# Kernel tuning notes

Hardware: AMD Instinct MI355X
Metric: run time of the kernel (lower is better)

The kernel has to match this reference:

```python
import jax, jax.numpy as jnp
import numpy as np

B, N, IN_DIM, DIM, HEADS, P = 4, 2048, 256, 512, 8, 16
DH = DIM // HEADS            # 64
SCALE = DH ** -0.5


def setup_inputs() -> dict:
    key = jax.random.key(0)
    ks = jax.random.split(key, 8)
    def w(k, shape, s=0.02):
        return jax.random.normal(k, shape, dtype=jnp.float32) * s
    return {
        "x": jax.random.normal(ks[0], (B, N, IN_DIM), dtype=jnp.float32),
        "w_qkv": w(ks[1], (IN_DIM, 3 * DIM)),
        "b_qkv": jnp.zeros((3 * DIM,), jnp.float32),
        "w_in": w(ks[2], (P, P)),
        "b_in": jnp.zeros((P,), jnp.float32),
        "w_out": w(ks[3], (P, P)),
        "b_out": jnp.zeros((P,), jnp.float32),
        "w_merge": w(ks[4], (DIM, DIM)),
        "b_merge": jnp.zeros((DIM,), jnp.float32),
        "w_proj": w(ks[5], (DIM + IN_DIM, DIM)),
        "b_proj": jnp.zeros((DIM,), jnp.float32),
        "H": 64,
        "W": 32,
    }


def reference(x, w_qkv, b_qkv, w_in, b_in, w_out, b_out,
              w_merge, b_merge, w_proj, b_proj, H, W):
    b, n, _ = x.shape
    qkv = x @ w_qkv + b_qkv                      # [b, n, 3*DIM]
    q, k, v = jnp.split(qkv, 3, axis=-1)
    def to_heads(t):
        return t.reshape(b, n, HEADS, DH).transpose(0, 2, 1, 3)  # [b, h, n, d]
    q, k, v = to_heads(q), to_heads(k), to_heads(v)
    # Original splits heads into h/v halves and runs two attentions, then
    # concats along the head axis. Softmax is per-head, so this is exactly
    # one batched multi-head attention with head order preserved.
    attn = jax.nn.softmax(jnp.einsum('bhnd,bhmd->bhnm', q, k) * SCALE, axis=-1)
    out = jnp.einsum('bhnm,bhmd->bhnd', attn, v)
    out = out.transpose(0, 2, 1, 3).reshape(b, n, DIM)
    out = out @ w_merge + b_merge
    # IBPP branch: view channels as [P, P] grid, linear-SiLU-linear on last dim
    xr = x.reshape(b, n, P, P)
    ib = jax.nn.silu(xr @ w_in + b_in) @ w_out + b_out
    ib = ib.reshape(b, n, IN_DIM)
    # proj (dropout p=0 -> identity)
    return jnp.concatenate([out, ib], axis=-1) @ w_proj + b_proj
```

## Files before the change

### kernel.cpp

```cpp
#include <hip/hip_runtime.h>


typedef unsigned short u16;
typedef unsigned int u32;
typedef __bf16 bf16x8 __attribute__((ext_vector_type(8)));
typedef u16 su16x8 __attribute__((ext_vector_type(8)));
typedef u16 su16x4 __attribute__((ext_vector_type(4)));
typedef u32 u32x4 __attribute__((ext_vector_type(4)));
typedef float f32x4 __attribute__((ext_vector_type(4)));
typedef float f32x16 __attribute__((ext_vector_type(16)));

__device__ __forceinline__ u16 f2bf(float f) {
  union { __bf16 h; u16 u; } v;
  v.h = (__bf16)f;
  return v.u;
}

__device__ __forceinline__ float fexp2(float x) {
#if __has_builtin(__builtin_amdgcn_exp2f)
  return __builtin_amdgcn_exp2f(x);
#else
  return __expf(x * 0.6931471805599453f);
#endif
}

__device__ __forceinline__ f32x4 zero4() {
  f32x4 v = {0.f, 0.f, 0.f, 0.f};
  return v;
}

__device__ __forceinline__ f32x4 mfma16(bf16x8 a, bf16x8 b, f32x4 c) {
  return __builtin_amdgcn_mfma_f32_16x16x32_bf16(a, b, c, 0, 0, 0);
}

__device__ __forceinline__ f32x16 mfma32(bf16x8 a, bf16x8 b, f32x16 c) {
  return __builtin_amdgcn_mfma_f32_32x32x16_bf16(a, b, c, 0, 0, 0);
}

__device__ __forceinline__ u32 pkbf(float a, float b) {
  u32 r;
  asm("v_cvt_pk_bf16_f32 %0, %1, %2" : "=v"(r) : "v"(a), "v"(b));
  return r;
}

__device__ __forceinline__ void swap32(u32& a, u32& b) {
  asm("v_permlane32_swap_b32 %0, %1" : "+v"(a), "+v"(b));
}

__device__ __forceinline__ bf16x8 mkfrag(u32 w0, u32 w1, u32 w2, u32 w3) {
  union { u32 u[4]; bf16x8 v; } x;
  x.u[0] = w0; x.u[1] = w1; x.u[2] = w2; x.u[3] = w3;
  return x.v;
}

__global__ __launch_bounds__(256) void prep_kernel(
    const float* __restrict__ w_qkv, const float* __restrict__ w_merge,
    const float* __restrict__ w_proj, const float* __restrict__ b_merge,
    const float* __restrict__ b_proj, u16* __restrict__ wqkvT,
    u16* __restrict__ wptT, u16* __restrict__ wcombT, u16* __restrict__ wmb,
    float* __restrict__ biasc) {
  int blk = blockIdx.x, tid = threadIdx.x;
  if (blk < 192) {
    const float* src;
    int lsrc, ldd, r0, c0;
    u16* dst;
    if (blk < 96) {
      src = w_qkv; lsrc = 1536; dst = wqkvT; ldd = 256;
      r0 = (blk & 3) * 64; c0 = (blk >> 2) * 64;
    } else if (blk < 160) {
      int b2 = blk - 96;
      src = w_proj; lsrc = 512; dst = wptT; ldd = 512;
      r0 = (b2 & 7) * 64; c0 = (b2 >> 3) * 64;
    } else {
      int b2 = blk - 160;
      src = w_proj + 512 * 512; lsrc = 512; dst = wcombT + 512; ldd = 768;
      r0 = (b2 & 3) * 64; c0 = (b2 >> 2) * 64;
    }
    __shared__ __align__(16) u16 Ts[64 * 68];
    int rr = tid >> 4, cc4 = (tid & 15) * 4;
#pragma unroll
    for (int rep = 0; rep < 4; ++rep) {
      int r = rr + rep * 16;
      float4 v = *(const float4*)&src[(size_t)(r0 + r) * lsrc + c0 + cc4];
      su16x4 pk = {f2bf(v.x), f2bf(v.y), f2bf(v.z), f2bf(v.w)};
      *(su16x4*)&Ts[r * 68 + cc4] = pk;
    }
    __syncthreads();
    int c = tid & 63, seg = tid >> 6;
    u16 tmp[16];
#pragma unroll
    for (int k = 0; k < 16; ++k) tmp[k] = Ts[(seg * 16 + k) * 68 + c];
    *(su16x8*)&dst[(size_t)(c0 + c) * ldd + r0 + seg * 16] = *(su16x8*)tmp;
    *(su16x8*)&dst[(size_t)(c0 + c) * ldd + r0 + seg * 16 + 8] =
        *(su16x8*)(tmp + 8);
  } else if (blk < 256) {
    int b2 = blk - 192;
#pragma unroll
    for (int rep = 0; rep < 4; ++rep) {
      int i = b2 * 4096 + rep * 1024 + tid * 4;
      float4 v = *(const float4*)&w_merge[i];
      su16x4 pk = {f2bf(v.x), f2bf(v.y), f2bf(v.z), f2bf(v.w)};
      *(su16x4*)&wmb[i] = pk;
    }
  } else {
    int col0 = (blk - 256) * 16;
    __shared__ float red[16][17];
    int kr = tid >> 4, cc = tid & 15;
    float s = 0.f;
#pragma unroll 4
    for (int j = 0; j < 32; ++j) {
      int k = kr + j * 16;
      s += b_merge[k] * w_proj[(size_t)k * 512 + col0 + cc];
    }
    red[kr][cc] = s;
    __syncthreads();
    if (kr == 0) {
      float a = b_proj[col0 + cc];
#pragma unroll
      for (int t = 0; t < 16; ++t) a += red[t][cc];
      biasc[col0 + cc] = a;
    }
  }
}

__global__ __launch_bounds__(256) void ib_kernel(
    const float* __restrict__ x, const float* __restrict__ w_in,
    const float* __restrict__ b_in, const float* __restrict__ w_out,
    const float* __restrict__ b_out, u16* __restrict__ xb,
    u16* __restrict__ catb) {
  __shared__ float wi[256], wo[256], bi[16], bo[16];
  __shared__ float xs[16][260];
  __shared__ float hs[16][260];
  int tid = threadIdx.x;
  wi[tid] = w_in[tid];
  wo[tid] = w_out[tid];
  if (tid < 16) { bi[tid] = b_in[tid]; bo[tid] = b_out[tid]; }
  size_t blkoff = (size_t)blockIdx.x * 4096;
#pragma unroll
  for (int i = 0; i < 4; ++i) {
    int f = (tid + i * 256) * 4;
    float4 v = *(const float4*)&x[blkoff + f];
    int tok = f >> 8, p = f & 255;
    *(float4*)&xs[tok][p] = v;
    su16x4 pk = {f2bf(v.x), f2bf(v.y), f2bf(v.z), f2bf(v.w)};
    *(su16x4*)&xb[blkoff + f] = pk;
  }
  __syncthreads();
  int t = tid >> 4, p2 = tid & 15;
#pragma unroll
  for (int p1 = 0; p1 < 16; ++p1) {
    float a = bi[p2];
#pragma unroll
    for (int k = 0; k < 16; ++k) a += xs[t][p1 * 16 + k] * wi[k * 16 + p2];
    hs[t][p1 * 16 + p2] = a / (1.f + __expf(-a));
  }
  __syncthreads();
  size_t tok = (size_t)blockIdx.x * 16 + t;
#pragma unroll
  for (int p1 = 0; p1 < 16; ++p1) {
    float o = bo[p2];
#pragma unroll
    for (int j = 0; j < 16; ++j) o += hs[t][p1 * 16 + j] * wo[j * 16 + p2];
    catb[tok * 768 + 512 + p1 * 16 + p2] = f2bf(o);
  }
}

template <int TM, int TN, int WGM, int WGN, int OUTMODE>
__global__ __launch_bounds__(256) void gemm_bt(
    const u16* __restrict__ A, int lda, const u16* __restrict__ BT, int ldb,
    int kcount, const float* __restrict__ bias, void* __restrict__ Co, int ldc,
    int scaleQ) {
  constexpr int NROWS = TM + TN;
  constexpr int NLD = NROWS / 64;
  constexpr int MT = TM / WGM / 16;
  constexpr int NT = TN / WGN / 16;
  __shared__ __align__(16) u16 S[NROWS * 40];
  int tid = threadIdx.x;
  int lane = tid & 63, wave = tid >> 6;
  int c = lane & 15, g4 = lane >> 4;
  int m0 = blockIdx.y * TM, n0 = blockIdx.x * TN;
  int wm = (wave / WGN) * (TM / WGM), wn = (wave % WGN) * (TN / WGN);
  f32x4 acc[MT][NT];
#pragma unroll
  for (int a = 0; a < MT; ++a)
#pragma unroll
    for (int b = 0; b < NT; ++b) acc[a][b] = zero4();

  su16x8 pre[NLD];
#pragma unroll
  for (int t = 0; t < NLD; ++t) {
    int gsl = t * 256 + tid;
    int row = gsl >> 2, kg = gsl & 3;
    const u16* p = row < TM ? &A[(size_t)(m0 + row) * lda + kg * 8]
                            : &BT[(size_t)(n0 + row - TM) * ldb + kg * 8];
    pre[t] = *(const su16x8*)p;
  }

  for (int kb = 0; kb < kcount; kb += 32) {
    __syncthreads();
#pragma unroll
    for (int t = 0; t < NLD; ++t) {
      int gsl = t * 256 + tid;
      int row = gsl >> 2, kg = gsl & 3;
      *(su16x8*)&S[row * 40 + kg * 8] = pre[t];
    }
    __syncthreads();
    if (kb + 32 < kcount) {
#pragma unroll
      for (int t = 0; t < NLD; ++t) {
        int gsl = t * 256 + tid;
        int row = gsl >> 2, kg = gsl & 3;
        const u16* p =
            row < TM ? &A[(size_t)(m0 + row) * lda + kb + 32 + kg * 8]
                     : &BT[(size_t)(n0 + row - TM) * ldb + kb + 32 + kg * 8];
        pre[t] = *(const su16x8*)p;
      }
    }
    bf16x8 af[MT], bf[NT];
#pragma unroll
    for (int mt = 0; mt < MT; ++mt)
      af[mt] = *(const bf16x8*)&S[(wm + mt * 16 + c) * 40 + g4 * 8];
#pragma unroll
    for (int nt = 0; nt < NT; ++nt)
      bf[nt] = *(const bf16x8*)&S[(TM + wn + nt * 16 + c) * 40 + g4 * 8];
#pragma unroll
    for (int mt = 0; mt < MT; ++mt)
#pragma unroll
      for (int nt = 0; nt < NT; ++nt)
        acc[mt][nt] = mfma16(af[mt], bf[nt], acc[mt][nt]);
  }

  if (OUTMODE == 0) {
    float* Cf = (float*)Co;
#pragma unroll
    for (int nt = 0; nt < NT; ++nt) {
      int col = n0 + wn + nt * 16 + c;
      float bv = bias ? bias[col] : 0.f;
#pragma unroll
      for (int mt = 0; mt < MT; ++mt)
#pragma unroll
        for (int i = 0; i < 4; ++i)
          Cf[(size_t)(m0 + wm + mt * 16 + g4 * 4 + i) * ldc + col] =
              acc[mt][nt][i] + bv;
    }
  } else if (OUTMODE == 2) {
    u16* C16 = (u16*)Co;
#pragma unroll
    for (int nt = 0; nt < NT; ++nt)
#pragma unroll
      for (int mt = 0; mt < MT; ++mt)
#pragma unroll
        for (int i = 0; i < 4; ++i)
          C16[(size_t)(m0 + wm + mt * 16 + g4 * 4 + i) * ldc + n0 + wn +
              nt * 16 + c] = f2bf(acc[mt][nt][i]);
  } else {
    u16* C16 = (u16*)Co;
    u16* Cs = S;
    __syncthreads();
#pragma unroll
    for (int half = 0; half < 2; ++half) {
      if ((wave >> 1) == half) {
#pragma unroll
        for (int nt = 0; nt < NT; ++nt) {
          int col = n0 + wn + nt * 16 + c;
          float bv = bias ? bias[col] : 0.f;
          float sc = (scaleQ && col < 512) ? 0.18033688011112042f : 1.f;
#pragma unroll
          for (int mt = 0; mt < MT; ++mt)
#pragma unroll
            for (int i = 0; i < 4; ++i)
              Cs[(mt * 16 + g4 * 4 + i) * 136 + wn + nt * 16 + c] =
                  f2bf((acc[mt][nt][i] + bv) * sc);
        }
      }
      __syncthreads();
      {
        int row = tid >> 2;
#pragma unroll
        for (int t = 0; t < 4; ++t) {
          int gr = (tid & 3) + t * 4;
          u32x4 v = *(const u32x4*)&Cs[row * 136 + gr * 8];
          *(u32x4*)&C16[(size_t)(m0 + half * 64 + row) * ldc + n0 + gr * 8] = v;
        }
      }
      __syncthreads();
    }
  }
}

__global__ __launch_bounds__(256, 2) void attn_kernel(
    const u16* __restrict__ qkvb, u16* __restrict__ catb) {
  __shared__ __align__(16) u16 Ks[2 * 9216];
  __shared__ __align__(16) u16 Vs[2 * 8704];
  int tid = threadIdx.x;
  int lane = tid & 63, wave = tid >> 6;
  int l31 = lane & 31, hi = lane >> 5;
  int wq = wave * 32;
  int bh = blockIdx.x & 31, qt = blockIdx.x >> 5;
  int bb = bh >> 3, h = bh & 7;
  size_t base = (size_t)bb * 2048 * 1536;

  bf16x8 qf[4];
  {
    int n = qt * 128 + wq + l31;
    const u16* qp = &qkvb[base + (size_t)n * 1536 + h * 64 + hi * 8];
#pragma unroll
    for (int kc = 0; kc < 4; ++kc) qf[kc] = *(const bf16x8*)(qp + kc * 16);
  }

  f32x16 oacc[2];
#pragma unroll
  for (int dt = 0; dt < 2; ++dt)
#pragma unroll
    for (int r = 0; r < 16; ++r) oacc[dt][r] = 0.f;
  float lsum = 0.f;

  su16x8 kpre[4], v0pre[2], v1pre[2];
  int kv_s = tid >> 3, dg_s = tid & 7;

  auto loadKV = [&](int n0k) {
#pragma unroll
    for (int t = 0; t < 4; ++t)
      kpre[t] = *(const su16x8*)&qkvb[base + (size_t)(n0k + kv_s + t * 32) *
                                                1536 +
                                      512 + h * 64 + dg_s * 8];
#pragma unroll
    for (int t = 0; t < 2; ++t) {
      const u16* vg = &qkvb[base + (size_t)(n0k + (kv_s + t * 32) * 2) * 1536 +
                            1024 + h * 64 + dg_s * 8];
      v0pre[t] = *(const su16x8*)vg;
      v1pre[t] = *(const su16x8*)(vg + 1536);
    }
  };

  auto stage = [&](int buf) {
    u16* ksw = Ks + buf * 9216;
    u32* vw = (u32*)(Vs + buf * 8704);
#pragma unroll
    for (int t = 0; t < 4; ++t)
      *(su16x8*)&ksw[(kv_s + t * 32) * 72 + dg_s * 8] = kpre[t];
#pragma unroll
    for (int t = 0; t < 2; ++t) {
      int kvp = kv_s + t * 32;
      int kvg = kvp >> 2, w2 = kvp & 3;
#pragma unroll
      for (int j = 0; j < 8; ++j) {
        int d = dg_s * 8 + j;
        vw[d * 68 + ((kvg ^ (dg_s & 3)) << 2) + w2] =
            (u32)v0pre[t][j] | ((u32)v1pre[t][j] << 16);
      }
    }
  };

  loadKV(0);
  stage(0);
  for (int kb2 = 0; kb2 < 16; ++kb2) {
    __syncthreads();
    int cur = kb2 & 1;
    if (kb2 < 15) loadKV((kb2 + 1) * 128);
    const u16* ksb = Ks + cur * 9216;
    const u16* vsb = Vs + cur * 8704;
#pragma unroll
    for (int kvt = 0; kvt < 4; ++kvt) {
      bf16x8 kf[4];
#pragma unroll
      for (int kc = 0; kc < 4; ++kc)
        kf[kc] =
            *(const bf16x8*)&ksb[(kvt * 32 + l31) * 72 + kc * 16 + hi * 8];
      f32x16 sacc;
#pragma unroll
      for (int r = 0; r < 16; ++r) sacc[r] = 0.f;
      __builtin_amdgcn_s_setprio(1);
#pragma unroll
      for (int kc = 0; kc < 4; ++kc) sacc = mfma32(kf[kc], qf[kc], sacc);
      __builtin_amdgcn_s_setprio(0);
      float p[16];
#pragma unroll
      for (int r = 0; r < 16; ++r) p[r] = fexp2(sacc[r]);
      lsum += ((((p[0] + p[1]) + (p[2] + p[3])) +
                ((p[4] + p[5]) + (p[6] + p[7]))) +
               (((p[8] + p[9]) + (p[10] + p[11])) +
                ((p[12] + p[13]) + (p[14] + p[15]))));
      u32 a0 = pkbf(p[0], p[1]), b0 = pkbf(p[4], p[5]);
      u32 a1 = pkbf(p[2], p[3]), b1 = pkbf(p[6], p[7]);
      u32 a2 = pkbf(p[8], p[9]), b2 = pkbf(p[12], p[13]);
      u32 a3 = pkbf(p[10], p[11]), b3 = pkbf(p[14], p[15]);
      swap32(a0, b0);
      swap32(a1, b1);
      swap32(a2, b2);
      swap32(a3, b3);
      bf16x8 pf0 = mkfrag(a0, a1, b0, b1);
      bf16x8 pf1 = mkfrag(a2, a3, b2, b3);
      __builtin_amdgcn_s_setprio(1);
#pragma unroll
      for (int kc2 = 0; kc2 < 2; ++kc2) {
        int g = (kvt * 2 + kc2) * 2 + hi;
#pragma unroll
        for (int dt = 0; dt < 2; ++dt) {
          int d = dt * 32 + l31;
          bf16x8 vf =
              *(const bf16x8*)&vsb[d * 136 + ((g ^ ((d >> 3) & 3)) << 3)];
          oacc[dt] = mfma32(kc2 ? pf1 : pf0, vf, oacc[dt]);
        }
      }
      __builtin_amdgcn_s_setprio(0);
    }
    if (kb2 < 15) stage(cur ^ 1);
  }
  lsum += __shfl_xor(lsum, 32);
#pragma unroll
  for (int r = 0; r < 16; ++r) {
    int qrow = (r & 3) + 8 * (r >> 2) + 4 * hi;
    float linv = 1.f / __shfl(lsum, qrow);
    size_t n = (size_t)(bb * 2048 + qt * 128 + wq + qrow);
    u16* cp = &catb[n * 768 + h * 64];
    cp[l31] = f2bf(oacc[0][r] * linv);
    cp[32 + l31] = f2bf(oacc[1][r] * linv);
  }
}

extern "C" void kernel_launch(void* const* d_in, const int* in_sizes, int n_in,
                              void* d_out, int out_size, void* d_ws,
                              size_t ws_size, hipStream_t stream) {
  const float* x = (const float*)d_in[0];
  const float* w_qkv = (const float*)d_in[1];
  const float* b_qkv = (const float*)d_in[2];
  const float* w_in = (const float*)d_in[3];
  const float* b_in = (const float*)d_in[4];
  const float* w_out = (const float*)d_in[5];
  const float* b_out = (const float*)d_in[6];
  const float* w_merge = (const float*)d_in[7];
  const float* b_merge = (const float*)d_in[8];
  const float* w_proj = (const float*)d_in[9];
  const float* b_proj = (const float*)d_in[10];

  char* ws = (char*)d_ws;
  u16* xb = (u16*)(ws + 0);
  u16* qkvb = (u16*)(ws + 4194304);
  u16* catb = (u16*)(ws + 29360128);
  u16* wqkvT = (u16*)(ws + 41943040);
  u16* wptT = (u16*)(ws + 42729472);
  u16* wmb = (u16*)(ws + 43253760);
  u16* wcombT = (u16*)(ws + 43778048);
  float* biasc = (float*)(ws + 44564480);

  prep_kernel<<<288, 256, 0, stream>>>(w_qkv, w_merge, w_proj, b_merge, b_proj,
                                       wqkvT, wptT, wcombT, wmb, biasc);
  ib_kernel<<<512, 256, 0, stream>>>(x, w_in, b_in, w_out, b_out, xb, catb);
  gemm_bt<128, 128, 2, 2, 1><<<dim3(12, 64), 256, 0, stream>>>(
      xb, 256, wqkvT, 256, 256, b_qkv, (void*)qkvb, 1536, 1);
  gemm_bt<64, 64, 2, 2, 2><<<dim3(8, 8), 256, 0, stream>>>(
      wptT, 512, wmb, 512, 512, nullptr, (void*)wcombT, 768, 0);
  attn_kernel<<<512, 256, 0, stream>>>(qkvb, catb);
  gemm_bt<128, 64, 4, 1, 0><<<dim3(8, 64), 256, 0, stream>>>(
      catb, 768, wcombT, 768, 768, biasc, d_out, 512, 0);
}
```

Baseline: 182.7 us.

## Split attention waves over query-pair and KV halves; merge prep and IBPP kernels

```diff
diff --git a/kernel.cpp b/kernel.cpp
--- a/kernel.cpp
+++ b/kernel.cpp
@@ -53,12 +53,16 @@
   return x.v;
 }
 
-__global__ __launch_bounds__(256) void prep_kernel(
+__global__ __launch_bounds__(256) void prep_ib_kernel(
     const float* __restrict__ w_qkv, const float* __restrict__ w_merge,
     const float* __restrict__ w_proj, const float* __restrict__ b_merge,
     const float* __restrict__ b_proj, u16* __restrict__ wqkvT,
     u16* __restrict__ wptT, u16* __restrict__ wcombT, u16* __restrict__ wmb,
-    float* __restrict__ biasc) {
+    float* __restrict__ biasc, const float* __restrict__ x,
+    const float* __restrict__ w_in, const float* __restrict__ b_in,
+    const float* __restrict__ w_out, const float* __restrict__ b_out,
+    u16* __restrict__ xb, u16* __restrict__ catb) {
+  __shared__ __align__(16) char smem[35456];
   int blk = blockIdx.x, tid = threadIdx.x;
   if (blk < 192) {
     const float* src;
@@ -76,7 +80,7 @@
       src = w_proj + 512 * 512; lsrc = 512; dst = wcombT + 512; ldd = 768;
       r0 = (b2 & 3) * 64; c0 = (b2 >> 2) * 64;
     }
-    __shared__ __align__(16) u16 Ts[64 * 68];
+    u16* Ts = (u16*)smem;
     int rr = tid >> 4, cc4 = (tid & 15) * 4;
 #pragma unroll
     for (int rep = 0; rep < 4; ++rep) {
@@ -102,9 +106,9 @@
       su16x4 pk = {f2bf(v.x), f2bf(v.y), f2bf(v.z), f2bf(v.w)};
       *(su16x4*)&wmb[i] = pk;
     }
-  } else {
+  } else if (blk < 288) {
     int col0 = (blk - 256) * 16;
-    __shared__ float red[16][17];
+    float(*red)[17] = (float(*)[17])smem;
     int kr = tid >> 4, cc = tid & 15;
     float s = 0.f;
 #pragma unroll 4
@@ -120,48 +124,45 @@
       for (int t = 0; t < 16; ++t) a += red[t][cc];
       biasc[col0 + cc] = a;
     }
-  }
-}
-
-__global__ __launch_bounds__(256) void ib_kernel(
-    const float* __restrict__ x, const float* __restrict__ w_in,
-    const float* __restrict__ b_in, const float* __restrict__ w_out,
-    const float* __restrict__ b_out, u16* __restrict__ xb,
-    u16* __restrict__ catb) {
-  __shared__ float wi[256], wo[256], bi[16], bo[16];
-  __shared__ float xs[16][260];
-  __shared__ float hs[16][260];
-  int tid = threadIdx.x;
-  wi[tid] = w_in[tid];
-  wo[tid] = w_out[tid];
-  if (tid < 16) { bi[tid] = b_in[tid]; bo[tid] = b_out[tid]; }
-  size_t blkoff = (size_t)blockIdx.x * 4096;
-#pragma unroll
-  for (int i = 0; i < 4; ++i) {
-    int f = (tid + i * 256) * 4;
-    float4 v = *(const float4*)&x[blkoff + f];
-    int tok = f >> 8, p = f & 255;
-    *(float4*)&xs[tok][p] = v;
-    su16x4 pk = {f2bf(v.x), f2bf(v.y), f2bf(v.z), f2bf(v.w)};
-    *(su16x4*)&xb[blkoff + f] = pk;
-  }
-  __syncthreads();
-  int t = tid >> 4, p2 = tid & 15;
-#pragma unroll
-  for (int p1 = 0; p1 < 16; ++p1) {
-    float a = bi[p2];
-#pragma unroll
-    for (int k = 0; k < 16; ++k) a += xs[t][p1 * 16 + k] * wi[k * 16 + p2];
-    hs[t][p1 * 16 + p2] = a / (1.f + __expf(-a));
-  }
-  __syncthreads();
-  size_t tok = (size_t)blockIdx.x * 16 + t;
-#pragma unroll
-  for (int p1 = 0; p1 < 16; ++p1) {
-    float o = bo[p2];
-#pragma unroll
-    for (int j = 0; j < 16; ++j) o += hs[t][p1 * 16 + j] * wo[j * 16 + p2];
-    catb[tok * 768 + 512 + p1 * 16 + p2] = f2bf(o);
+  } else {
+    int ib = blk - 288;
+    float* wi = (float*)smem;
+    float* wo = (float*)(smem + 1024);
+    float* bi = (float*)(smem + 2048);
+    float* bo = (float*)(smem + 2112);
+    float(*xs)[260] = (float(*)[260])(smem + 2176);
+    float(*hs)[260] = (float(*)[260])(smem + 18816);
+    wi[tid] = w_in[tid];
+    wo[tid] = w_out[tid];
+    if (tid < 16) { bi[tid] = b_in[tid]; bo[tid] = b_out[tid]; }
+    size_t blkoff = (size_t)ib * 4096;
+#pragma unroll
+    for (int i = 0; i < 4; ++i) {
+      int f = (tid + i * 256) * 4;
+      float4 v = *(const float4*)&x[blkoff + f];
+      int tok = f >> 8, p = f & 255;
+      *(float4*)&xs[tok][p] = v;
+      su16x4 pk = {f2bf(v.x), f2bf(v.y), f2bf(v.z), f2bf(v.w)};
+      *(su16x4*)&xb[blkoff + f] = pk;
+    }
+    __syncthreads();
+    int t = tid >> 4, p2 = tid & 15;
+#pragma unroll
+    for (int p1 = 0; p1 < 16; ++p1) {
+      float a = bi[p2];
+#pragma unroll
+      for (int k = 0; k < 16; ++k) a += xs[t][p1 * 16 + k] * wi[k * 16 + p2];
+      hs[t][p1 * 16 + p2] = a / (1.f + __expf(-a));
+    }
+    __syncthreads();
+    size_t tok = (size_t)ib * 16 + t;
+#pragma unroll
+    for (int p1 = 0; p1 < 16; ++p1) {
+      float o = bo[p2];
+#pragma unroll
+      for (int j = 0; j < 16; ++j) o += hs[t][p1 * 16 + j] * wo[j * 16 + p2];
+      catb[tok * 768 + 512 + p1 * 16 + p2] = f2bf(o);
+    }
   }
 }
 
@@ -295,25 +296,28 @@
   int tid = threadIdx.x;
   int lane = tid & 63, wave = tid >> 6;
   int l31 = lane & 31, hi = lane >> 5;
-  int wq = wave * 32;
+  int qh = wave >> 1, kh = wave & 1;
   int bh = blockIdx.x & 31, qt = blockIdx.x >> 5;
   int bb = bh >> 3, h = bh & 7;
   size_t base = (size_t)bb * 2048 * 1536;
 
-  bf16x8 qf[4];
-  {
-    int n = qt * 128 + wq + l31;
+  bf16x8 qf[2][4];
+#pragma unroll
+  for (int qg = 0; qg < 2; ++qg) {
+    int n = qt * 128 + qh * 64 + qg * 32 + l31;
     const u16* qp = &qkvb[base + (size_t)n * 1536 + h * 64 + hi * 8];
 #pragma unroll
-    for (int kc = 0; kc < 4; ++kc) qf[kc] = *(const bf16x8*)(qp + kc * 16);
-  }
-
-  f32x16 oacc[2];
-#pragma unroll
-  for (int dt = 0; dt < 2; ++dt)
-#pragma unroll
-    for (int r = 0; r < 16; ++r) oacc[dt][r] = 0.f;
-  float lsum = 0.f;
+    for (int kc = 0; kc < 4; ++kc) qf[qg][kc] = *(const bf16x8*)(qp + kc * 16);
+  }
+
+  f32x16 oacc[2][2];
+#pragma unroll
+  for (int qg = 0; qg < 2; ++qg)
+#pragma unroll
+    for (int dt = 0; dt < 2; ++dt)
+#pragma unroll
+      for (int r = 0; r < 16; ++r) oacc[qg][dt][r] = 0.f;
+  float lsum[2] = {0.f, 0.f};
 
   su16x8 kpre[4], v0pre[2], v1pre[2];
   int kv_s = tid >> 3, dg_s = tid & 7;
@@ -346,7 +350,7 @@
 #pragma unroll
       for (int j = 0; j < 8; ++j) {
         int d = dg_s * 8 + j;
-        vw[d * 68 + ((kvg ^ (dg_s & 3)) << 2) + w2] =
+        vw[d * 68 + ((kvg ^ (dg_s & 7)) << 2) + w2] =
             (u32)v0pre[t][j] | ((u32)v1pre[t][j] << 16);
       }
     }
@@ -361,61 +365,97 @@
     const u16* ksb = Ks + cur * 9216;
     const u16* vsb = Vs + cur * 8704;
 #pragma unroll
-    for (int kvt = 0; kvt < 4; ++kvt) {
+    for (int kvt = 0; kvt < 2; ++kvt) {
       bf16x8 kf[4];
 #pragma unroll
       for (int kc = 0; kc < 4; ++kc)
-        kf[kc] =
-            *(const bf16x8*)&ksb[(kvt * 32 + l31) * 72 + kc * 16 + hi * 8];
-      f32x16 sacc;
-#pragma unroll
-      for (int r = 0; r < 16; ++r) sacc[r] = 0.f;
+        kf[kc] = *(const bf16x8*)&ksb[(kh * 64 + kvt * 32 + l31) * 72 +
+                                      kc * 16 + hi * 8];
+      f32x16 s0, s1;
+#pragma unroll
+      for (int r = 0; r < 16; ++r) { s0[r] = 0.f; s1[r] = 0.f; }
       __builtin_amdgcn_s_setprio(1);
 #pragma unroll
-      for (int kc = 0; kc < 4; ++kc) sacc = mfma32(kf[kc], qf[kc], sacc);
+      for (int kc = 0; kc < 4; ++kc) {
+        s0 = mfma32(kf[kc], qf[0][kc], s0);
+        s1 = mfma32(kf[kc], qf[1][kc], s1);
+      }
       __builtin_amdgcn_s_setprio(0);
-      float p[16];
-#pragma unroll
-      for (int r = 0; r < 16; ++r) p[r] = fexp2(sacc[r]);
-      lsum += ((((p[0] + p[1]) + (p[2] + p[3])) +
-                ((p[4] + p[5]) + (p[6] + p[7]))) +
-               (((p[8] + p[9]) + (p[10] + p[11])) +
-                ((p[12] + p[13]) + (p[14] + p[15]))));
-      u32 a0 = pkbf(p[0], p[1]), b0 = pkbf(p[4], p[5]);
-      u32 a1 = pkbf(p[2], p[3]), b1 = pkbf(p[6], p[7]);
-      u32 a2 = pkbf(p[8], p[9]), b2 = pkbf(p[12], p[13]);
-      u32 a3 = pkbf(p[10], p[11]), b3 = pkbf(p[14], p[15]);
-      swap32(a0, b0);
-      swap32(a1, b1);
-      swap32(a2, b2);
-      swap32(a3, b3);
-      bf16x8 pf0 = mkfrag(a0, a1, b0, b1);
-      bf16x8 pf1 = mkfrag(a2, a3, b2, b3);
+      bf16x8 pf[2][2];
+#pragma unroll
+      for (int qg = 0; qg < 2; ++qg) {
+        float p[16];
+#pragma unroll
+        for (int r = 0; r < 16; ++r) p[r] = fexp2(qg ? s1[r] : s0[r]);
+        lsum[qg] += ((((p[0] + p[1]) + (p[2] + p[3])) +
+                      ((p[4] + p[5]) + (p[6] + p[7]))) +
+                     (((p[8] + p[9]) + (p[10] + p[11])) +
+                      ((p[12] + p[13]) + (p[14] + p[15]))));
+        u32 a0 = pkbf(p[0], p[1]), b0 = pkbf(p[4], p[5]);
+        u32 a1 = pkbf(p[2], p[3]), b1 = pkbf(p[6], p[7]);
+        u32 a2 = pkbf(p[8], p[9]), b2 = pkbf(p[12], p[13]);
+        u32 a3 = pkbf(p[10], p[11]), b3 = pkbf(p[14], p[15]);
+        swap32(a0, b0);
+        swap32(a1, b1);
+        swap32(a2, b2);
+        swap32(a3, b3);
+        pf[qg][0] = mkfrag(a0, a1, b0, b1);
+        pf[qg][1] = mkfrag(a2, a3, b2, b3);
+      }
       __builtin_amdgcn_s_setprio(1);
 #pragma unroll
       for (int kc2 = 0; kc2 < 2; ++kc2) {
-        int g = (kvt * 2 + kc2) * 2 + hi;
+        int g = kh * 8 + (kvt * 2 + kc2) * 2 + hi;
 #pragma unroll
         for (int dt = 0; dt < 2; ++dt) {
           int d = dt * 32 + l31;
           bf16x8 vf =
-              *(const bf16x8*)&vsb[d * 136 + ((g ^ ((d >> 3) & 3)) << 3)];
-          oacc[dt] = mfma32(kc2 ? pf1 : pf0, vf, oacc[dt]);
+              *(const bf16x8*)&vsb[d * 136 + ((g ^ ((d >> 3) & 7)) << 3)];
+          oacc[0][dt] = mfma32(pf[0][kc2], vf, oacc[0][dt]);
+          oacc[1][dt] = mfma32(pf[1][kc2], vf, oacc[1][dt]);
         }
       }
       __builtin_amdgcn_s_setprio(0);
     }
     if (kb2 < 15) stage(cur ^ 1);
   }
-  lsum += __shfl_xor(lsum, 32);
-#pragma unroll
-  for (int r = 0; r < 16; ++r) {
-    int qrow = (r & 3) + 8 * (r >> 2) + 4 * hi;
-    float linv = 1.f / __shfl(lsum, qrow);
-    size_t n = (size_t)(bb * 2048 + qt * 128 + wq + qrow);
-    u16* cp = &catb[n * 768 + h * 64];
-    cp[l31] = f2bf(oacc[0][r] * linv);
-    cp[32 + l31] = f2bf(oacc[1][r] * linv);
+#pragma unroll
+  for (int qg = 0; qg < 2; ++qg) lsum[qg] += __shfl_xor(lsum[qg], 32);
+
+  __syncthreads();
+  float* Of = (float*)Ks;
+  float* Lf = (float*)Vs;
+  if (kh == 1) {
+#pragma unroll
+    for (int qg = 0; qg < 2; ++qg) {
+#pragma unroll
+      for (int dt = 0; dt < 2; ++dt)
+#pragma unroll
+        for (int r = 0; r < 16; ++r) {
+          int qrow = (r & 3) + 8 * (r >> 2) + 4 * hi;
+          Of[(qh * 64 + qg * 32 + qrow) * 68 + dt * 32 + l31] = oacc[qg][dt][r];
+        }
+      if (hi == 0) Lf[qh * 64 + qg * 32 + l31] = lsum[qg];
+    }
+  }
+  __syncthreads();
+  if (kh == 0) {
+#pragma unroll
+    for (int qg = 0; qg < 2; ++qg) {
+      float lt = lsum[qg] + Lf[qh * 64 + qg * 32 + l31];
+#pragma unroll
+      for (int r = 0; r < 16; ++r) {
+        int qrow = (r & 3) + 8 * (r >> 2) + 4 * hi;
+        float linv = 1.f / __shfl(lt, qrow);
+        int qq = qh * 64 + qg * 32 + qrow;
+        float o0 = oacc[qg][0][r] + Of[qq * 68 + l31];
+        float o1 = oacc[qg][1][r] + Of[qq * 68 + 32 + l31];
+        size_t n = (size_t)(bb * 2048 + qt * 128 + qq);
+        u16* cp = &catb[n * 768 + h * 64];
+        cp[l31] = f2bf(o0 * linv);
+        cp[32 + l31] = f2bf(o1 * linv);
+      }
+    }
   }
 }
 
@@ -444,9 +484,10 @@
   u16* wcombT = (u16*)(ws + 43778048);
   float* biasc = (float*)(ws + 44564480);
 
-  prep_kernel<<<288, 256, 0, stream>>>(w_qkv, w_merge, w_proj, b_merge, b_proj,
-                                       wqkvT, wptT, wcombT, wmb, biasc);
-  ib_kernel<<<512, 256, 0, stream>>>(x, w_in, b_in, w_out, b_out, xb, catb);
+  prep_ib_kernel<<<800, 256, 0, stream>>>(w_qkv, w_merge, w_proj, b_merge,
+                                          b_proj, wqkvT, wptT, wcombT, wmb,
+                                          biasc, x, w_in, b_in, w_out, b_out,
+                                          xb, catb);
   gemm_bt<128, 128, 2, 2, 1><<<dim3(12, 64), 256, 0, stream>>>(
       xb, 256, wqkvT, 256, 256, b_qkv, (void*)qkvb, 1536, 1);
   gemm_bt<64, 64, 2, 2, 2><<<dim3(8, 8), 256, 0, stream>>>(
```

Result: no change. 182.5 us (-0.1%).

## Merge weight prep and IBPP kernels into one launch; widen V smem swizzle

Applied to the files above, without the earlier changes.

```diff
diff --git a/kernel.cpp b/kernel.cpp
--- a/kernel.cpp
+++ b/kernel.cpp
@@ -53,12 +53,16 @@
   return x.v;
 }
 
-__global__ __launch_bounds__(256) void prep_kernel(
+__global__ __launch_bounds__(256) void prep_ib_kernel(
     const float* __restrict__ w_qkv, const float* __restrict__ w_merge,
     const float* __restrict__ w_proj, const float* __restrict__ b_merge,
     const float* __restrict__ b_proj, u16* __restrict__ wqkvT,
     u16* __restrict__ wptT, u16* __restrict__ wcombT, u16* __restrict__ wmb,
-    float* __restrict__ biasc) {
+    float* __restrict__ biasc, const float* __restrict__ x,
+    const float* __restrict__ w_in, const float* __restrict__ b_in,
+    const float* __restrict__ w_out, const float* __restrict__ b_out,
+    u16* __restrict__ xb, u16* __restrict__ catb) {
+  __shared__ __align__(16) char smem[35456];
   int blk = blockIdx.x, tid = threadIdx.x;
   if (blk < 192) {
     const float* src;
@@ -76,7 +80,7 @@
       src = w_proj + 512 * 512; lsrc = 512; dst = wcombT + 512; ldd = 768;
       r0 = (b2 & 3) * 64; c0 = (b2 >> 2) * 64;
     }
-    __shared__ __align__(16) u16 Ts[64 * 68];
+    u16* Ts = (u16*)smem;
     int rr = tid >> 4, cc4 = (tid & 15) * 4;
 #pragma unroll
     for (int rep = 0; rep < 4; ++rep) {
@@ -102,9 +106,9 @@
       su16x4 pk = {f2bf(v.x), f2bf(v.y), f2bf(v.z), f2bf(v.w)};
       *(su16x4*)&wmb[i] = pk;
     }
-  } else {
+  } else if (blk < 288) {
     int col0 = (blk - 256) * 16;
-    __shared__ float red[16][17];
+    float(*red)[17] = (float(*)[17])smem;
     int kr = tid >> 4, cc = tid & 15;
     float s = 0.f;
 #pragma unroll 4
@@ -120,48 +124,45 @@
       for (int t = 0; t < 16; ++t) a += red[t][cc];
       biasc[col0 + cc] = a;
     }
-  }
-}
-
-__global__ __launch_bounds__(256) void ib_kernel(
-    const float* __restrict__ x, const float* __restrict__ w_in,
-    const float* __restrict__ b_in, const float* __restrict__ w_out,
-    const float* __restrict__ b_out, u16* __restrict__ xb,
-    u16* __restrict__ catb) {
-  __shared__ float wi[256], wo[256], bi[16], bo[16];
-  __shared__ float xs[16][260];
-  __shared__ float hs[16][260];
-  int tid = threadIdx.x;
-  wi[tid] = w_in[tid];
-  wo[tid] = w_out[tid];
-  if (tid < 16) { bi[tid] = b_in[tid]; bo[tid] = b_out[tid]; }
-  size_t blkoff = (size_t)blockIdx.x * 4096;
-#pragma unroll
-  for (int i = 0; i < 4; ++i) {
-    int f = (tid + i * 256) * 4;
-    float4 v = *(const float4*)&x[blkoff + f];
-    int tok = f >> 8, p = f & 255;
-    *(float4*)&xs[tok][p] = v;
-    su16x4 pk = {f2bf(v.x), f2bf(v.y), f2bf(v.z), f2bf(v.w)};
-    *(su16x4*)&xb[blkoff + f] = pk;
-  }
-  __syncthreads();
-  int t = tid >> 4, p2 = tid & 15;
-#pragma unroll
-  for (int p1 = 0; p1 < 16; ++p1) {
-    float a = bi[p2];
-#pragma unroll
-    for (int k = 0; k < 16; ++k) a += xs[t][p1 * 16 + k] * wi[k * 16 + p2];
-    hs[t][p1 * 16 + p2] = a / (1.f + __expf(-a));
-  }
-  __syncthreads();
-  size_t tok = (size_t)blockIdx.x * 16 + t;
-#pragma unroll
-  for (int p1 = 0; p1 < 16; ++p1) {
-    float o = bo[p2];
-#pragma unroll
-    for (int j = 0; j < 16; ++j) o += hs[t][p1 * 16 + j] * wo[j * 16 + p2];
-    catb[tok * 768 + 512 + p1 * 16 + p2] = f2bf(o);
+  } else {
+    int ib = blk - 288;
+    float* wi = (float*)smem;
+    float* wo = (float*)(smem + 1024);
+    float* bi = (float*)(smem + 2048);
+    float* bo = (float*)(smem + 2112);
+    float(*xs)[260] = (float(*)[260])(smem + 2176);
+    float(*hs)[260] = (float(*)[260])(smem + 18816);
+    wi[tid] = w_in[tid];
+    wo[tid] = w_out[tid];
+    if (tid < 16) { bi[tid] = b_in[tid]; bo[tid] = b_out[tid]; }
+    size_t blkoff = (size_t)ib * 4096;
+#pragma unroll
+    for (int i = 0; i < 4; ++i) {
+      int f = (tid + i * 256) * 4;
+      float4 v = *(const float4*)&x[blkoff + f];
+      int tok = f >> 8, p = f & 255;
+      *(float4*)&xs[tok][p] = v;
+      su16x4 pk = {f2bf(v.x), f2bf(v.y), f2bf(v.z), f2bf(v.w)};
+      *(su16x4*)&xb[blkoff + f] = pk;
+    }
+    __syncthreads();
+    int t = tid >> 4, p2 = tid & 15;
+#pragma unroll
+    for (int p1 = 0; p1 < 16; ++p1) {
+      float a = bi[p2];
+#pragma unroll
+      for (int k = 0; k < 16; ++k) a += xs[t][p1 * 16 + k] * wi[k * 16 + p2];
+      hs[t][p1 * 16 + p2] = a / (1.f + __expf(-a));
+    }
+    __syncthreads();
+    size_t tok = (size_t)ib * 16 + t;
+#pragma unroll
+    for (int p1 = 0; p1 < 16; ++p1) {
+      float o = bo[p2];
+#pragma unroll
+      for (int j = 0; j < 16; ++j) o += hs[t][p1 * 16 + j] * wo[j * 16 + p2];
+      catb[tok * 768 + 512 + p1 * 16 + p2] = f2bf(o);
+    }
   }
 }
 
@@ -346,7 +347,7 @@
 #pragma unroll
       for (int j = 0; j < 8; ++j) {
         int d = dg_s * 8 + j;
-        vw[d * 68 + ((kvg ^ (dg_s & 3)) << 2) + w2] =
+        vw[d * 68 + ((kvg ^ (dg_s & 7)) << 2) + w2] =
             (u32)v0pre[t][j] | ((u32)v1pre[t][j] << 16);
       }
     }
@@ -399,7 +400,7 @@
         for (int dt = 0; dt < 2; ++dt) {
           int d = dt * 32 + l31;
           bf16x8 vf =
-              *(const bf16x8*)&vsb[d * 136 + ((g ^ ((d >> 3) & 3)) << 3)];
+              *(const bf16x8*)&vsb[d * 136 + ((g ^ ((d >> 3) & 7)) << 3)];
           oacc[dt] = mfma32(kc2 ? pf1 : pf0, vf, oacc[dt]);
         }
       }
@@ -444,9 +445,10 @@
   u16* wcombT = (u16*)(ws + 43778048);
   float* biasc = (float*)(ws + 44564480);
 
-  prep_kernel<<<288, 256, 0, stream>>>(w_qkv, w_merge, w_proj, b_merge, b_proj,
-                                       wqkvT, wptT, wcombT, wmb, biasc);
-  ib_kernel<<<512, 256, 0, stream>>>(x, w_in, b_in, w_out, b_out, xb, catb);
+  prep_ib_kernel<<<800, 256, 0, stream>>>(w_qkv, w_merge, w_proj, b_merge,
+                                          b_proj, wqkvT, wptT, wcombT, wmb,
+                                          biasc, x, w_in, b_in, w_out, b_out,
+                                          xb, catb);
   gemm_bt<128, 128, 2, 2, 1><<<dim3(12, 64), 256, 0, stream>>>(
       xb, 256, wqkvT, 256, 256, b_qkv, (void*)qkvb, 1536, 1);
   gemm_bt<64, 64, 2, 2, 2><<<dim3(8, 8), 256, 0, stream>>>(
```

Result: faster. 175.9 us (-3.7%).
